# Kernel tuning notes

Measured on AMD Instinct MI355X. Metric: run time of the kernel, lower is better.

The kernel has to match this reference:

```python
import jax, jax.numpy as jnp
import numpy as np

N, P, M, J, H = 32768, 5, 1024, 24, 256
SMPL_THRESH = 0.08


def _rand_transforms(rng, n):
    # random small-angle rotations + small translations -> invertible 4x4 joint transforms
    axis = rng.normal(size=(n, 3))
    axis /= np.linalg.norm(axis, axis=-1, keepdims=True)
    ang = rng.uniform(-0.5, 0.5, size=(n, 1, 1))
    K = np.zeros((n, 3, 3))
    K[:, 0, 1] = -axis[:, 2]; K[:, 0, 2] = axis[:, 1]
    K[:, 1, 0] = axis[:, 2];  K[:, 1, 2] = -axis[:, 0]
    K[:, 2, 0] = -axis[:, 1]; K[:, 2, 1] = axis[:, 0]
    R = np.eye(3)[None] + np.sin(ang) * K + (1.0 - np.cos(ang)) * (K @ K)
    T = np.zeros((n, 4, 4))
    T[:, :3, :3] = R
    T[:, :3, 3] = rng.normal(size=(n, 3)) * 0.1
    T[:, 3, 3] = 1.0
    return T.astype(np.float32)


def setup_inputs() -> dict:
    key = jax.random.key(0)
    ks = jax.random.split(key, 12)
    rng = np.random.default_rng(0)
    pose_pts = jax.random.normal(ks[0], (1, N, 3), jnp.float32) * 0.5
    pose_dirs = jax.random.normal(ks[1], (1, N, 3), jnp.float32)
    pose_dirs = pose_dirs / jnp.linalg.norm(pose_dirs, axis=-1, keepdims=True)
    part_pts = jax.random.normal(ks[2], (P, M, 3), jnp.float32) * 0.5
    part_pbw = jax.nn.softmax(jax.random.normal(ks[3], (P, M, J), jnp.float32), axis=-1)
    A = jnp.asarray(_rand_transforms(rng, J))[None]       # [1,24,4,4]
    big_A = jnp.asarray(_rand_transforms(rng, J))[None]   # [1,24,4,4]
    W1 = jax.random.normal(ks[4], (3, H), jnp.float32) * 0.1
    b1 = jnp.zeros((H,), jnp.float32)
    W2 = jax.random.normal(ks[5], (H, H), jnp.float32) * 0.06
    b2 = jnp.zeros((H,), jnp.float32)
    W3 = jax.random.normal(ks[6], (H, 3), jnp.float32) * 0.06
    b3 = jnp.zeros((3,), jnp.float32)
    lengths2 = jnp.full((P,), M, dtype=jnp.int32)
    return {"pose_pts": pose_pts, "pose_dirs": pose_dirs, "part_pts": part_pts,
            "part_pbw": part_pbw, "A": A, "big_A": big_A,
            "W1": W1, "b1": b1, "W2": W2, "b2": b2, "W3": W3, "b3": b3,
            "lengths2": lengths2}


def _lbs_pipeline(pose_pts, pose_dirs, part_pts, part_pbw, A, big_A,
                  W1, b1, W2, b2, W3, b3, lengths2):
    # ---- KNN (K=1) blend-weight lookup per part (torch.no_grad block) ----
    x = pose_pts[0]                                              # [N,3]
    d2 = (jnp.sum(x * x, -1)[:, None, None]
          - 2.0 * jnp.einsum('nd,pmd->npm', x, part_pts)
          + jnp.sum(part_pts * part_pts, -1)[None])              # [N,P,M]
    valid = jnp.arange(M)[None, :] < lengths2[:, None]           # [P,M]
    d2 = jnp.where(valid[None], jnp.maximum(d2, 0.0), jnp.inf)
    nn = jnp.argmin(d2, axis=-1)                                 # [N,P]
    pnorm = jnp.sqrt(jnp.take_along_axis(d2, nn[..., None], -1)[..., 0])  # [N,P]
    bw = part_pbw[jnp.arange(P)[None, :], nn]                    # [N,P,24]
    bw = jax.lax.stop_gradient(bw)
    pnorm = jax.lax.stop_gradient(pnorm)
    pflag = pnorm < SMPL_THRESH                                  # [N,P]

    # ---- gather-expand: each point assigned to every part ----
    pts_e = jnp.broadcast_to(x[:, None, :], (N, P, 3)).reshape(N * P, 3)
    dirs_e = jnp.broadcast_to(pose_dirs[0][:, None, :], (N, P, 3)).reshape(N * P, 3)
    bw_f = bw.reshape(N * P, J)

    # ---- per-point inverse linear blend skinning ----
    A_bw = jnp.einsum('kj,jxy->kxy', bw_f, A[0])                 # [NP,4,4]
    R_inv = jnp.linalg.inv(A_bw[:, :3, :3])
    tpts = jnp.einsum('kxy,ky->kx', R_inv, pts_e - A_bw[:, :3, 3])
    Ab = jnp.einsum('kj,jxy->kxy', bw_f, big_A[0])               # [NP,4,4]
    Rb = Ab[:, :3, :3]
    init_bigpose = jnp.einsum('kxy,ky->kx', Rb, tpts) + Ab[:, :3, 3]
    tdirs = jnp.einsum('kxy,ky->kx', R_inv, dirs_e)
    tpose_dirs = jnp.einsum('kxy,ky->kx', Rb, tdirs).reshape(1, N, P, 3)

    # ---- tpose deformer (residual MLP, masked by part flag) ----
    h = jax.nn.relu(init_bigpose @ W1 + b1)
    h = jax.nn.relu(h @ W2 + b2)
    resd = 0.05 * jnp.tanh(h @ W3 + b3)
    resd = resd * pflag.reshape(N * P, 1).astype(resd.dtype)
    tpose = (init_bigpose + resd).reshape(1, N, P, 3)
    return (tpose, tpose_dirs, resd.reshape(1, N, P, 3),
            pflag.reshape(1, N, P), init_bigpose[None], pnorm[None])


def reference(pose_pts, pose_dirs, part_pts, part_pbw, A, big_A,
              W1, b1, W2, b2, W3, b3, lengths2):
    return _lbs_pipeline(pose_pts, pose_dirs, part_pts, part_pbw, A, big_A,
                         W1, b1, W2, b2, W3, b3, lengths2)
```

## Files before the change

kernel.cpp:

```cpp
#include <hip/hip_runtime.h>
#include <stdint.h>
#include <math.h>

#define NPTS 32768
#define PP   5
#define MM   1024
#define JJ   24
#define HH   256

#define O0 0
#define O1 491520
#define O2 983040
#define O3 1474560
#define O4 1638400
#define O5 2129920

typedef unsigned short ushort_t;
typedef unsigned int   uint_t;
typedef unsigned long long u64_t;
typedef __attribute__((ext_vector_type(8))) short bf16x8;
typedef __attribute__((ext_vector_type(4))) float f32x4;
typedef __attribute__((ext_vector_type(2))) float f32x2;

__device__ __forceinline__ ushort_t f2bf(float f) {
  union { uint_t i; float f; } v; v.f = f;
  uint_t i = v.i;
  return (ushort_t)((i + 0x7FFFu + ((i >> 16) & 1u)) >> 16);
}
__device__ __forceinline__ uint_t cvt_pk_bf16(float lo, float hi) {
  uint_t r;
  asm("v_cvt_pk_bf16_f32 %0, %1, %2" : "=v"(r) : "v"(lo), "v"(hi));
  return r;
}
__device__ __forceinline__ float tanh_fast(float v) {
  v = fminf(fmaxf(v, -15.f), 15.f);
  float e = __expf(2.f*v);
  return __fdividef(e - 1.f, e + 1.f);
}
__device__ __forceinline__ float dpp_sum16(float x) {
  x += __int_as_float(__builtin_amdgcn_update_dpp(0, __float_as_int(x), 0x108, 0xF, 0xF, true));
  x += __int_as_float(__builtin_amdgcn_update_dpp(0, __float_as_int(x), 0x104, 0xF, 0xF, true));
  x += __int_as_float(__builtin_amdgcn_update_dpp(0, __float_as_int(x), 0x102, 0xF, 0xF, true));
  x += __int_as_float(__builtin_amdgcn_update_dpp(0, __float_as_int(x), 0x101, 0xF, 0xF, true));
  return x;
}

__device__ __forceinline__ void transform_one(
    int n, int p, int nn, float pn, float fl,
    float px, float py, float pz, float dx, float dy, float dz,
    const float* __restrict__ pbw,
    const float4* __restrict__ sA4, const float4* __restrict__ sB4,
    float* __restrict__ out)
{
  const float4* bwr = (const float4*)(pbw + ((size_t)p * MM + nn) * JJ);
  float bw[24];
  #pragma unroll
  for (int q = 0; q < 6; ++q) {
    float4 u = bwr[q];
    bw[q*4+0] = u.x; bw[q*4+1] = u.y; bw[q*4+2] = u.z; bw[q*4+3] = u.w;
  }

  float M1[12], M2[12];
  #pragma unroll
  for (int q = 0; q < 12; ++q) { M1[q] = 0.f; M2[q] = 0.f; }
  #pragma unroll
  for (int j = 0; j < 24; ++j) {
    float w = bw[j];
    float4 a0 = sA4[j*3+0], a1 = sA4[j*3+1], a2 = sA4[j*3+2];
    M1[0]=fmaf(w,a0.x,M1[0]); M1[1]=fmaf(w,a0.y,M1[1]); M1[2]=fmaf(w,a0.z,M1[2]); M1[3]=fmaf(w,a0.w,M1[3]);
    M1[4]=fmaf(w,a1.x,M1[4]); M1[5]=fmaf(w,a1.y,M1[5]); M1[6]=fmaf(w,a1.z,M1[6]); M1[7]=fmaf(w,a1.w,M1[7]);
    M1[8]=fmaf(w,a2.x,M1[8]); M1[9]=fmaf(w,a2.y,M1[9]); M1[10]=fmaf(w,a2.z,M1[10]); M1[11]=fmaf(w,a2.w,M1[11]);
    float4 c0 = sB4[j*3+0], c1 = sB4[j*3+1], c2 = sB4[j*3+2];
    M2[0]=fmaf(w,c0.x,M2[0]); M2[1]=fmaf(w,c0.y,M2[1]); M2[2]=fmaf(w,c0.z,M2[2]); M2[3]=fmaf(w,c0.w,M2[3]);
    M2[4]=fmaf(w,c1.x,M2[4]); M2[5]=fmaf(w,c1.y,M2[5]); M2[6]=fmaf(w,c1.z,M2[6]); M2[7]=fmaf(w,c1.w,M2[7]);
    M2[8]=fmaf(w,c2.x,M2[8]); M2[9]=fmaf(w,c2.y,M2[9]); M2[10]=fmaf(w,c2.z,M2[10]); M2[11]=fmaf(w,c2.w,M2[11]);
  }
  float a=M1[0], b=M1[1], c=M1[2];
  float d=M1[4], e=M1[5], f=M1[6];
  float g=M1[8], h=M1[9], i=M1[10];
  float C00 = e*i - f*h, C01 = c*h - b*i, C02 = b*f - c*e;
  float C10 = f*g - d*i, C11 = a*i - c*g, C12 = c*d - a*f;
  float C20 = d*h - e*g, C21 = b*g - a*h, C22 = a*e - b*d;
  float det = a*C00 + b*C10 + c*C20;
  float rd = 1.0f / det;
  float tx = px - M1[3], ty = py - M1[7], tz = pz - M1[11];
  float t0 = rd * (C00*tx + C01*ty + C02*tz);
  float t1 = rd * (C10*tx + C11*ty + C12*tz);
  float t2 = rd * (C20*tx + C21*ty + C22*tz);
  float i0 = M2[0]*t0 + M2[1]*t1 + M2[2]*t2  + M2[3];
  float i1 = M2[4]*t0 + M2[5]*t1 + M2[6]*t2  + M2[7];
  float i2 = M2[8]*t0 + M2[9]*t1 + M2[10]*t2 + M2[11];
  float d0 = rd * (C00*dx + C01*dy + C02*dz);
  float d1 = rd * (C10*dx + C11*dy + C12*dz);
  float d2 = rd * (C20*dx + C21*dy + C22*dz);
  float e0 = M2[0]*d0 + M2[1]*d1 + M2[2]*d2;
  float e1 = M2[4]*d0 + M2[5]*d1 + M2[6]*d2;
  float e2 = M2[8]*d0 + M2[9]*d1 + M2[10]*d2;

  size_t k = (size_t)n * PP + p;
  out[O1 + k*3+0] = e0; out[O1 + k*3+1] = e1; out[O1 + k*3+2] = e2;
  out[O3 + k] = fl;
  out[O4 + k*3+0] = i0; out[O4 + k*3+1] = i1; out[O4 + k*3+2] = i2;
  out[O5 + k] = pn;
}

__global__ __launch_bounds__(256) void nn_kernel(
    const float* __restrict__ pp0, const float* __restrict__ pp1,
    const float* __restrict__ part_pts, const float* __restrict__ pbw,
    const float* __restrict__ Ag, const float* __restrict__ Bg,
    const int* __restrict__ lengths2,
    const float* __restrict__ W2g, ushort_t* __restrict__ W2bf,
    float* __restrict__ out)
{
  if (blockIdx.x >= 1280) {
    int k = blockIdx.x - 1280;
    int n = threadIdx.x;
    float v = W2g[k*256 + n];
    int kc = k >> 5, quad = (k & 31) >> 3, j = k & 7;
    int tile = n >> 4, lane = quad*16 + (n & 15);
    W2bf[kc*8192 + tile*512 + lane*8 + j] = f2bf(v);
    return;
  }

  __shared__ float4 sXq[256], sYq[256], sZq[256], sWq[256];
  __shared__ float4 sA4[72];
  __shared__ float4 sB4[72];
  int t = threadIdx.x;
  int p  = blockIdx.x >> 8;
  int nb = blockIdx.x & 255;
  int g  = t >> 3;
  int s  = t & 7;
  int n0 = nb*128 + g*4;

  float s0r0 = pp0[0], s0r1 = pp0[1], s0r2 = pp0[2];
  float nrm = s0r0*s0r0 + s0r1*s0r1 + s0r2*s0r2;
  bool c0_is_dirs = fabsf(nrm - 1.0f) < 1e-4f;
  const float* pose_pts  = c0_is_dirs ? pp1 : pp0;
  const float* pose_dirs = c0_is_dirs ? pp0 : pp1;

  {
    #pragma clang fp contract(off)
    float* fX = (float*)sXq; float* fY = (float*)sYq;
    float* fZ = (float*)sZq; float* fW = (float*)sWq;
    for (int i = t; i < MM; i += 256) {
      float x = part_pts[((size_t)p*MM+i)*3+0];
      float y = part_pts[((size_t)p*MM+i)*3+1];
      float z = part_pts[((size_t)p*MM+i)*3+2];
      float yy = ((x*x) + (y*y)) + (z*z);
      fX[i] = x; fY[i] = y; fZ[i] = z; fW[i] = yy;
    }
  }
  for (int i = t; i < 72; i += 256) {
    int l = i*4;
    int j = l / 12, rc = l % 12;
    float4 qa, qb;
    qa.x = Ag[j*16+rc+0]; qa.y = Ag[j*16+rc+1]; qa.z = Ag[j*16+rc+2]; qa.w = Ag[j*16+rc+3];
    qb.x = Bg[j*16+rc+0]; qb.y = Bg[j*16+rc+1]; qb.z = Bg[j*16+rc+2]; qb.w = Bg[j*16+rc+3];
    sA4[i] = qa; sB4[i] = qb;
  }
  int mlen = lengths2[p]; if (mlen > MM) mlen = MM;
  __syncthreads();

  float X[4], Y[4], Z[4];
  f32x2 Xd[4], Yd[4], Zd[4], C2[4];
  {
    #pragma clang fp contract(off)
    const float4* pr = (const float4*)(pose_pts + (size_t)n0*3);
    float4 f0 = pr[0], f1 = pr[1], f2 = pr[2];
    X[0]=f0.x; Y[0]=f0.y; Z[0]=f0.z;
    X[1]=f0.w; Y[1]=f1.x; Z[1]=f1.y;
    X[2]=f1.z; Y[2]=f1.w; Z[2]=f2.x;
    X[3]=f2.y; Y[3]=f2.z; Z[3]=f2.w;
    #pragma unroll
    for (int j = 0; j < 4; ++j) {
      float x2 = ((X[j]*X[j]) + (Y[j]*Y[j])) + (Z[j]*Z[j]);
      Xd[j] = (f32x2){2.0f*X[j], 2.0f*X[j]};
      Yd[j] = (f32x2){2.0f*Y[j], 2.0f*Y[j]};
      Zd[j] = (f32x2){2.0f*Z[j], 2.0f*Z[j]};
      C2[j] = (f32x2){x2, x2};
    }
  }

  float best[4]  = {INFINITY, INFINITY, INFINITY, INFINITY};
  int   kb[4]    = {0, 0, 0, 0};
  int   mbest[4] = {0, 0, 0, 0};
  int   nq = mlen >> 5;
  {
    #pragma clang fp contract(off)
    for (int k = 0; k < nq; ++k) {
      int qi = k*8 + s;
      float4 QX = sXq[qi], QY = sYq[qi], QZ = sZq[qi], QW = sWq[qi];
      f32x2 qx0 = {QX.x, QX.y}, qx1 = {QX.z, QX.w};
      f32x2 qy0 = {QY.x, QY.y}, qy1 = {QY.z, QY.w};
      f32x2 qz0 = {QZ.x, QZ.y}, qz1 = {QZ.z, QZ.w};
      f32x2 qw0 = {QW.x, QW.y}, qw1 = {QW.z, QW.w};
      #pragma unroll
      for (int j = 0; j < 4; ++j) {
        f32x2 dt0 = ((Xd[j]*qx0) + (Yd[j]*qy0)) + (Zd[j]*qz0);
        f32x2 tt0 = (C2[j] - dt0) + qw0;
        f32x2 dt1 = ((Xd[j]*qx1) + (Yd[j]*qy1)) + (Zd[j]*qz1);
        f32x2 tt1 = (C2[j] - dt1) + qw1;
        float e0 = fmaxf(tt0.x, 0.f);
        float e1 = fmaxf(tt0.y, 0.f);
        float e2 = fmaxf(tt1.x, 0.f);
        float e3 = fmaxf(tt1.y, 0.f);
        float m01 = fminf(e0, e1);
        float m23 = fminf(e2, e3);
        float lmin = fminf(m01, m23);
        bool lt = lmin < best[j];
        best[j] = fminf(best[j], lmin);
        kb[j] = lt ? k : kb[j];
      }
    }
    if (nq > 0) {
      #pragma unroll
      for (int j = 0; j < 4; ++j) {
        int qi = kb[j]*8 + s;
        float4 QX = sXq[qi], QY = sYq[qi], QZ = sZq[qi], QW = sWq[qi];
        float dA = ((Xd[j].x*QX.x) + (Yd[j].x*QY.x)) + (Zd[j].x*QZ.x);
        float eA = fmaxf((C2[j].x - dA) + QW.x, 0.f);
        float dB = ((Xd[j].x*QX.y) + (Yd[j].x*QY.y)) + (Zd[j].x*QZ.y);
        float eB = fmaxf((C2[j].x - dB) + QW.y, 0.f);
        float dC = ((Xd[j].x*QX.z) + (Yd[j].x*QY.z)) + (Zd[j].x*QZ.z);
        float eC = fmaxf((C2[j].x - dC) + QW.z, 0.f);
        int e = (eA == best[j]) ? 0 : (eB == best[j]) ? 1 : (eC == best[j]) ? 2 : 3;
        mbest[j] = (kb[j] << 5) + 4*s + e;
      }
    } else {
      #pragma unroll
      for (int j = 0; j < 4; ++j) mbest[j] = 4*s;
    }
    int mb0 = nq << 5;
    if (mb0 < mlen) {
      const float* fX = (const float*)sXq; const float* fY = (const float*)sYq;
      const float* fZ = (const float*)sZq; const float* fW = (const float*)sWq;
      #pragma unroll
      for (int e = 0; e < 4; ++e) {
        int m = mb0 + 4*s + e;
        if (m < mlen) {
          float qx = fX[m], qy = fY[m], qz = fZ[m], qw = fW[m];
          #pragma unroll
          for (int j = 0; j < 4; ++j) {
            float dt2 = ((Xd[j].x*qx) + (Yd[j].x*qy)) + (Zd[j].x*qz);
            float dd = fmaxf((C2[j].x - dt2) + qw, 0.0f);
            bool lt = dd < best[j];
            best[j] = fminf(best[j], dd);
            mbest[j] = lt ? m : mbest[j];
          }
        }
      }
    }
  }

  u64_t pk[4];
  #pragma unroll
  for (int j = 0; j < 4; ++j) {
    pk[j] = ((u64_t)__float_as_uint(best[j]) << 32) | (uint_t)mbest[j];
    u64_t o;
    o = __shfl_xor(pk[j], 1); if (o < pk[j]) pk[j] = o;
    o = __shfl_xor(pk[j], 2); if (o < pk[j]) pk[j] = o;
    o = __shfl_xor(pk[j], 4); if (o < pk[j]) pk[j] = o;
  }

  if (s < 4) {
    u64_t mypk = (s==0) ? pk[0] : (s==1) ? pk[1] : (s==2) ? pk[2] : pk[3];
    float xa = (s==0) ? X[0] : (s==1) ? X[1] : (s==2) ? X[2] : X[3];
    float ya = (s==0) ? Y[0] : (s==1) ? Y[1] : (s==2) ? Y[2] : Y[3];
    float za = (s==0) ? Z[0] : (s==1) ? Z[1] : (s==2) ? Z[2] : Z[3];
    int n = n0 + s;
    int bm = (int)(mypk & 0xFFFFFFFFull);
    float bd = __uint_as_float((uint_t)(mypk >> 32));
    float pn = sqrtf(bd);
    float fl = ((double)pn < 0.08) ? 1.0f : 0.0f;
    float dxa = pose_dirs[n*3+0], dya = pose_dirs[n*3+1], dza = pose_dirs[n*3+2];
    transform_one(n, p, bm, pn, fl, xa, ya, za, dxa, dya, dza, pbw, sA4, sB4, out);
  }
}

__global__ __launch_bounds__(256) void mlp_kernel(
    const float* __restrict__ W1g, const float* __restrict__ b1g,
    const float* __restrict__ b2g, const float* __restrict__ W3g,
    const float* __restrict__ b3g, const ushort_t* __restrict__ W2bf,
    float* __restrict__ out)
{
  __shared__ __align__(16) char smem[25088];
  ushort_t* sH   = (ushort_t*)smem;
  float4*   w1c  = (float4*)(smem + 16384);
  float4*   w3b2 = (float4*)(smem + 20480);
  float4*   sRow = (float4*)(smem + 24576);
  float*    prt  = (float*)smem;

  int t = threadIdx.x;
  int wave = t >> 6, lane = t & 63, quad = lane >> 4, m16 = lane & 15;
  size_t row0 = (size_t)blockIdx.x * 128;

  {
    int c = t;
    w1c[c]  = make_float4(W1g[c], W1g[256+c], W1g[512+c], b1g[c]);
    w3b2[c] = make_float4(W3g[c*3+0], W3g[c*3+1], W3g[c*3+2], b2g[c]);
  }

  #pragma unroll 1
  for (int pass = 0; pass < 4; ++pass) {
    size_t rbase = row0 + pass*32;
    if (t < 32) {
      size_t r = rbase + t;
      sRow[t] = make_float4(out[O4 + r*3+0], out[O4 + r*3+1], out[O4 + r*3+2],
                            out[O3 + r]);
    }
    __syncthreads();

    {
      int q8 = t & 31, rg = t >> 5;
      int kcw = q8 >> 2, qd = q8 & 3;
      int c0 = kcw*32 + qd*8;
      float4 wv[8];
      #pragma unroll
      for (int j = 0; j < 8; ++j) wv[j] = w1c[c0 + j];
      #pragma unroll
      for (int rr = 0; rr < 4; ++rr) {
        int r = rg*4 + rr;
        float4 xyz = sRow[r];
        uint_t u0, u1, u2, u3;
        {
          float4 wA = wv[0], wB = wv[1];
          float hA = fmaxf(fmaf(xyz.z, wA.z, fmaf(xyz.y, wA.y, fmaf(xyz.x, wA.x, wA.w))), 0.f);
          float hB = fmaxf(fmaf(xyz.z, wB.z, fmaf(xyz.y, wB.y, fmaf(xyz.x, wB.x, wB.w))), 0.f);
          u0 = cvt_pk_bf16(hA, hB);
        }
        {
          float4 wA = wv[2], wB = wv[3];
          float hA = fmaxf(fmaf(xyz.z, wA.z, fmaf(xyz.y, wA.y, fmaf(xyz.x, wA.x, wA.w))), 0.f);
          float hB = fmaxf(fmaf(xyz.z, wB.z, fmaf(xyz.y, wB.y, fmaf(xyz.x, wB.x, wB.w))), 0.f);
          u1 = cvt_pk_bf16(hA, hB);
        }
        {
          float4 wA = wv[4], wB = wv[5];
          float hA = fmaxf(fmaf(xyz.z, wA.z, fmaf(xyz.y, wA.y, fmaf(xyz.x, wA.x, wA.w))), 0.f);
          float hB = fmaxf(fmaf(xyz.z, wB.z, fmaf(xyz.y, wB.y, fmaf(xyz.x, wB.x, wB.w))), 0.f);
          u2 = cvt_pk_bf16(hA, hB);
        }
        {
          float4 wA = wv[6], wB = wv[7];
          float hA = fmaxf(fmaf(xyz.z, wA.z, fmaf(xyz.y, wA.y, fmaf(xyz.x, wA.x, wA.w))), 0.f);
          float hB = fmaxf(fmaf(xyz.z, wB.z, fmaf(xyz.y, wB.y, fmaf(xyz.x, wB.x, wB.w))), 0.f);
          u3 = cvt_pk_bf16(hA, hB);
        }
        int mt = r >> 4, r15 = r & 15;
        int l = qd*16 + r15;
        *(uint4*)(&sH[((mt*8 + kcw)*64 + l)*8]) = make_uint4(u0, u1, u2, u3);
      }
    }
    __syncthreads();

    const ushort_t* Wlane = W2bf + (size_t)wave*2048 + lane*8;
    bf16x8 Bcur[4], Bnxt[4];
    #pragma unroll
    for (int q = 0; q < 4; ++q) Bcur[q] = *(const bf16x8*)(Wlane + q*512);

    f32x4 acc[8];
    #pragma unroll
    for (int i = 0; i < 8; ++i) acc[i] = (f32x4){0.f,0.f,0.f,0.f};

    #pragma unroll 1
    for (int kc = 0; kc < 8; ++kc) {
      bf16x8 Af[2];
      #pragma unroll
      for (int mt = 0; mt < 2; ++mt)
        Af[mt] = *(const bf16x8*)(&sH[((mt*8 + kc)*64 + lane)*8]);
      if (kc < 7) {
        #pragma unroll
        for (int q = 0; q < 4; ++q)
          Bnxt[q] = *(const bf16x8*)(Wlane + (kc+1)*8192 + q*512);
      }
      #pragma unroll
      for (int mt = 0; mt < 2; ++mt)
        #pragma unroll
        for (int q = 0; q < 4; ++q)
          acc[mt*4+q] = __builtin_amdgcn_mfma_f32_16x16x32_bf16(Af[mt], Bcur[q], acc[mt*4+q], 0, 0, 0);
      if (kc < 7) {
        #pragma unroll
        for (int q = 0; q < 4; ++q) Bcur[q] = Bnxt[q];
      }
    }
    __syncthreads();

    float4 cvq[4];
    #pragma unroll
    for (int q = 0; q < 4; ++q) cvq[q] = w3b2[(wave*4+q)*16 + m16];

    #pragma unroll
    for (int mt = 0; mt < 2; ++mt) {
      #pragma unroll
      for (int reg = 0; reg < 4; ++reg) {
        float q0 = 0.f, q1 = 0.f, q2 = 0.f;
        #pragma unroll
        for (int q = 0; q < 4; ++q) {
          float h2 = fmaxf(acc[mt*4+q][reg] + cvq[q].w, 0.f);
          q0 = fmaf(h2, cvq[q].x, q0);
          q1 = fmaf(h2, cvq[q].y, q1);
          q2 = fmaf(h2, cvq[q].z, q2);
        }
        q0 = dpp_sum16(q0);
        q1 = dpp_sum16(q1);
        q2 = dpp_sum16(q2);
        if (m16 == 0) {
          int lr = mt*16 + quad*4 + reg;
          prt[(lr*4 + wave)*3 + 0] = q0;
          prt[(lr*4 + wave)*3 + 1] = q1;
          prt[(lr*4 + wave)*3 + 2] = q2;
        }
      }
    }
    __syncthreads();

    if (t < 128) {
      int lr = t >> 2, c = t & 3;
      if (c < 3) {
        float v = ((prt[(lr*4+0)*3+c] + prt[(lr*4+1)*3+c]) + prt[(lr*4+2)*3+c]) + prt[(lr*4+3)*3+c];
        size_t r = rbase + lr;
        float4 ib = sRow[lr];
        float iv = (c == 0) ? ib.x : (c == 1) ? ib.y : ib.z;
        float rr = 0.05f * tanh_fast(v + b3g[c]) * ib.w;
        out[O0 + r*3 + c] = iv + rr;
        out[O2 + r*3 + c] = rr;
      }
    }
    __syncthreads();
  }
}

extern "C" void kernel_launch(void* const* d_in, const int* in_sizes, int n_in,
                              void* d_out, int out_size, void* d_ws, size_t ws_size,
                              hipStream_t stream) {
  (void)out_size; (void)ws_size;
  const int want[13] = {98304, 98304, 15360, 122880, 384, 384, 768, 256, 65536, 256, 768, 3, 5};
  int idx[13];
  bool used[64] = {false};
  for (int L = 0; L < 13; ++L) {
    idx[L] = -1;
    for (int s = 0; s < n_in && s < 64; ++s) {
      if (!used[s] && in_sizes[s] == want[L]) { idx[L] = s; used[s] = true; break; }
    }
    if (idx[L] < 0) idx[L] = L;
  }
  const float* pp0       = (const float*)d_in[idx[0]];
  const float* pp1       = (const float*)d_in[idx[1]];
  const float* part_pts  = (const float*)d_in[idx[2]];
  const float* part_pbw  = (const float*)d_in[idx[3]];
  const float* A         = (const float*)d_in[idx[4]];
  const float* bigA      = (const float*)d_in[idx[5]];
  const float* W1        = (const float*)d_in[idx[6]];
  const float* b1        = (const float*)d_in[idx[7]];
  const float* W2        = (const float*)d_in[idx[8]];
  const float* b2        = (const float*)d_in[idx[9]];
  const float* W3        = (const float*)d_in[idx[10]];
  const float* b3        = (const float*)d_in[idx[11]];
  const int*   lengths2  = (const int*)d_in[idx[12]];
  float* out = (float*)d_out;
  ushort_t* W2bf = (ushort_t*)d_ws;

  nn_kernel<<<1536, 256, 0, stream>>>(pp0, pp1, part_pts, part_pbw,
                                      A, bigA, lengths2, W2, W2bf, out);
  mlp_kernel<<<1280, 256, 0, stream>>>(W1, b1, b2, W3, b3, W2bf, out);
}
```

Measured before the change: 170.2 us.

## Process 64 rows per MLP block in one pass instead of four 32-row passes

The MLP kernel now handles 64 rows per block in a single pass rather than looping over four 32-row passes of a 128-row block, and the grid doubles to 2560 blocks. Each W2 fragment loaded from global memory now feeds four M-tiles instead of two, doubling reuse per load, and the per-pass barriers are removed. The layer-1 compute is re-mapped so each thread handles one row and eight column groups. The cost is 16 accumulator vectors per thread, which raises register pressure, and more blocks each reloading W1/W3 into shared memory.

```diff
diff --git a/kernel.cpp b/kernel.cpp
--- a/kernel.cpp
+++ b/kernel.cpp
@@ -283,150 +283,138 @@
     const float* __restrict__ b3g, const ushort_t* __restrict__ W2bf,
     float* __restrict__ out)
 {
-  __shared__ __align__(16) char smem[25088];
-  ushort_t* sH   = (ushort_t*)smem;
-  float4*   w1c  = (float4*)(smem + 16384);
-  float4*   w3b2 = (float4*)(smem + 20480);
-  float4*   sRow = (float4*)(smem + 24576);
-  float*    prt  = (float*)smem;
+  __shared__ ushort_t sH[4*8*512];
+  __shared__ float4 w1c[256];
+  __shared__ float4 w3b2[256];
+  __shared__ float4 sRow[64];
+  __shared__ float  prt[64][4][3];
 
   int t = threadIdx.x;
   int wave = t >> 6, lane = t & 63, quad = lane >> 4, m16 = lane & 15;
-  size_t row0 = (size_t)blockIdx.x * 128;
+  size_t row0 = (size_t)blockIdx.x * 64;
 
   {
     int c = t;
     w1c[c]  = make_float4(W1g[c], W1g[256+c], W1g[512+c], b1g[c]);
     w3b2[c] = make_float4(W3g[c*3+0], W3g[c*3+1], W3g[c*3+2], b2g[c]);
-  }
-
-  #pragma unroll 1
-  for (int pass = 0; pass < 4; ++pass) {
-    size_t rbase = row0 + pass*32;
-    if (t < 32) {
-      size_t r = rbase + t;
+    if (t < 64) {
+      size_t r = row0 + t;
       sRow[t] = make_float4(out[O4 + r*3+0], out[O4 + r*3+1], out[O4 + r*3+2],
                             out[O3 + r]);
     }
-    __syncthreads();
-
-    {
-      int q8 = t & 31, rg = t >> 5;
-      int kcw = q8 >> 2, qd = q8 & 3;
+  }
+  __syncthreads();
+
+  {
+    int r = t & 63;
+    float4 xyz = sRow[r];
+    int mt = r >> 4, r15 = r & 15;
+    #pragma unroll
+    for (int j = 0; j < 8; ++j) {
+      int o = wave*8 + j;
+      int kcw = o >> 2, qd = o & 3;
       int c0 = kcw*32 + qd*8;
-      float4 wv[8];
-      #pragma unroll
-      for (int j = 0; j < 8; ++j) wv[j] = w1c[c0 + j];
-      #pragma unroll
-      for (int rr = 0; rr < 4; ++rr) {
-        int r = rg*4 + rr;
-        float4 xyz = sRow[r];
-        uint_t u0, u1, u2, u3;
-        {
-          float4 wA = wv[0], wB = wv[1];
-          float hA = fmaxf(fmaf(xyz.z, wA.z, fmaf(xyz.y, wA.y, fmaf(xyz.x, wA.x, wA.w))), 0.f);
-          float hB = fmaxf(fmaf(xyz.z, wB.z, fmaf(xyz.y, wB.y, fmaf(xyz.x, wB.x, wB.w))), 0.f);
-          u0 = cvt_pk_bf16(hA, hB);
-        }
-        {
-          float4 wA = wv[2], wB = wv[3];
-          float hA = fmaxf(fmaf(xyz.z, wA.z, fmaf(xyz.y, wA.y, fmaf(xyz.x, wA.x, wA.w))), 0.f);
-          float hB = fmaxf(fmaf(xyz.z, wB.z, fmaf(xyz.y, wB.y, fmaf(xyz.x, wB.x, wB.w))), 0.f);
-          u1 = cvt_pk_bf16(hA, hB);
-        }
-        {
-          float4 wA = wv[4], wB = wv[5];
-          float hA = fmaxf(fmaf(xyz.z, wA.z, fmaf(xyz.y, wA.y, fmaf(xyz.x, wA.x, wA.w))), 0.f);
-          float hB = fmaxf(fmaf(xyz.z, wB.z, fmaf(xyz.y, wB.y, fmaf(xyz.x, wB.x, wB.w))), 0.f);
-          u2 = cvt_pk_bf16(hA, hB);
-        }
-        {
-          float4 wA = wv[6], wB = wv[7];
-          float hA = fmaxf(fmaf(xyz.z, wA.z, fmaf(xyz.y, wA.y, fmaf(xyz.x, wA.x, wA.w))), 0.f);
-          float hB = fmaxf(fmaf(xyz.z, wB.z, fmaf(xyz.y, wB.y, fmaf(xyz.x, wB.x, wB.w))), 0.f);
-          u3 = cvt_pk_bf16(hA, hB);
-        }
-        int mt = r >> 4, r15 = r & 15;
-        int l = qd*16 + r15;
-        *(uint4*)(&sH[((mt*8 + kcw)*64 + l)*8]) = make_uint4(u0, u1, u2, u3);
-      }
-    }
-    __syncthreads();
-
-    const ushort_t* Wlane = W2bf + (size_t)wave*2048 + lane*8;
-    bf16x8 Bcur[4], Bnxt[4];
+      uint_t u0, u1, u2, u3;
+      {
+        float4 wA = w1c[c0 + 0], wB = w1c[c0 + 1];
+        float hA = fmaxf(fmaf(xyz.z, wA.z, fmaf(xyz.y, wA.y, fmaf(xyz.x, wA.x, wA.w))), 0.f);
+        float hB = fmaxf(fmaf(xyz.z, wB.z, fmaf(xyz.y, wB.y, fmaf(xyz.x, wB.x, wB.w))), 0.f);
+        u0 = cvt_pk_bf16(hA, hB);
+      }
+      {
+        float4 wA = w1c[c0 + 2], wB = w1c[c0 + 3];
+        float hA = fmaxf(fmaf(xyz.z, wA.z, fmaf(xyz.y, wA.y, fmaf(xyz.x, wA.x, wA.w))), 0.f);
+        float hB = fmaxf(fmaf(xyz.z, wB.z, fmaf(xyz.y, wB.y, fmaf(xyz.x, wB.x, wB.w))), 0.f);
+        u1 = cvt_pk_bf16(hA, hB);
+      }
+      {
+        float4 wA = w1c[c0 + 4], wB = w1c[c0 + 5];
+        float hA = fmaxf(fmaf(xyz.z, wA.z, fmaf(xyz.y, wA.y, fmaf(xyz.x, wA.x, wA.w))), 0.f);
+        float hB = fmaxf(fmaf(xyz.z, wB.z, fmaf(xyz.y, wB.y, fmaf(xyz.x, wB.x, wB.w))), 0.f);
+        u2 = cvt_pk_bf16(hA, hB);
+      }
+      {
+        float4 wA = w1c[c0 + 6], wB = w1c[c0 + 7];
+        float hA = fmaxf(fmaf(xyz.z, wA.z, fmaf(xyz.y, wA.y, fmaf(xyz.x, wA.x, wA.w))), 0.f);
+        float hB = fmaxf(fmaf(xyz.z, wB.z, fmaf(xyz.y, wB.y, fmaf(xyz.x, wB.x, wB.w))), 0.f);
+        u3 = cvt_pk_bf16(hA, hB);
+      }
+      *(uint4*)(&sH[((mt*8 + kcw)*64 + qd*16 + r15)*8]) = make_uint4(u0, u1, u2, u3);
+    }
+  }
+  __syncthreads();
+
+  const ushort_t* Wlane = W2bf + (size_t)wave*2048 + lane*8;
+  bf16x8 Bcur[4], Bnxt[4];
+  #pragma unroll
+  for (int q = 0; q < 4; ++q) Bcur[q] = *(const bf16x8*)(Wlane + q*512);
+
+  f32x4 acc[16];
+  #pragma unroll
+  for (int i = 0; i < 16; ++i) acc[i] = (f32x4){0.f,0.f,0.f,0.f};
+
+  #pragma unroll 1
+  for (int kc = 0; kc < 8; ++kc) {
+    bf16x8 Af[4];
     #pragma unroll
-    for (int q = 0; q < 4; ++q) Bcur[q] = *(const bf16x8*)(Wlane + q*512);
-
-    f32x4 acc[8];
+    for (int mt = 0; mt < 4; ++mt)
+      Af[mt] = *(const bf16x8*)(&sH[((mt*8 + kc)*64 + lane)*8]);
+    if (kc < 7) {
+      #pragma unroll
+      for (int q = 0; q < 4; ++q)
+        Bnxt[q] = *(const bf16x8*)(Wlane + (kc+1)*8192 + q*512);
+    }
     #pragma unroll
-    for (int i = 0; i < 8; ++i) acc[i] = (f32x4){0.f,0.f,0.f,0.f};
-
-    #pragma unroll 1
-    for (int kc = 0; kc < 8; ++kc) {
-      bf16x8 Af[2];
-      #pragma unroll
-      for (int mt = 0; mt < 2; ++mt)
-        Af[mt] = *(const bf16x8*)(&sH[((mt*8 + kc)*64 + lane)*8]);
-      if (kc < 7) {
-        #pragma unroll
-        for (int q = 0; q < 4; ++q)
-          Bnxt[q] = *(const bf16x8*)(Wlane + (kc+1)*8192 + q*512);
-      }
-      #pragma unroll
-      for (int mt = 0; mt < 2; ++mt)
-        #pragma unroll
-        for (int q = 0; q < 4; ++q)
-          acc[mt*4+q] = __builtin_amdgcn_mfma_f32_16x16x32_bf16(Af[mt], Bcur[q], acc[mt*4+q], 0, 0, 0);
-      if (kc < 7) {
-        #pragma unroll
-        for (int q = 0; q < 4; ++q) Bcur[q] = Bnxt[q];
-      }
-    }
-    __syncthreads();
-
-    float4 cvq[4];
+    for (int mt = 0; mt < 4; ++mt)
+      #pragma unroll
+      for (int q = 0; q < 4; ++q)
+        acc[mt*4+q] = __builtin_amdgcn_mfma_f32_16x16x32_bf16(Af[mt], Bcur[q], acc[mt*4+q], 0, 0, 0);
+    if (kc < 7) {
+      #pragma unroll
+      for (int q = 0; q < 4; ++q) Bcur[q] = Bnxt[q];
+    }
+  }
+
+  float4 cvq[4];
+  #pragma unroll
+  for (int q = 0; q < 4; ++q) cvq[q] = w3b2[(wave*4+q)*16 + m16];
+
+  #pragma unroll
+  for (int mt = 0; mt < 4; ++mt) {
     #pragma unroll
-    for (int q = 0; q < 4; ++q) cvq[q] = w3b2[(wave*4+q)*16 + m16];
-
-    #pragma unroll
-    for (int mt = 0; mt < 2; ++mt) {
-      #pragma unroll
-      for (int reg = 0; reg < 4; ++reg) {
-        float q0 = 0.f, q1 = 0.f, q2 = 0.f;
-        #pragma unroll
-        for (int q = 0; q < 4; ++q) {
-          float h2 = fmaxf(acc[mt*4+q][reg] + cvq[q].w, 0.f);
-          q0 = fmaf(h2, cvq[q].x, q0);
-          q1 = fmaf(h2, cvq[q].y, q1);
-          q2 = fmaf(h2, cvq[q].z, q2);
-        }
-        q0 = dpp_sum16(q0);
-        q1 = dpp_sum16(q1);
-        q2 = dpp_sum16(q2);
-        if (m16 == 0) {
-          int lr = mt*16 + quad*4 + reg;
-          prt[(lr*4 + wave)*3 + 0] = q0;
-          prt[(lr*4 + wave)*3 + 1] = q1;
-          prt[(lr*4 + wave)*3 + 2] = q2;
-        }
-      }
-    }
-    __syncthreads();
-
-    if (t < 128) {
-      int lr = t >> 2, c = t & 3;
-      if (c < 3) {
-        float v = ((prt[(lr*4+0)*3+c] + prt[(lr*4+1)*3+c]) + prt[(lr*4+2)*3+c]) + prt[(lr*4+3)*3+c];
-        size_t r = rbase + lr;
-        float4 ib = sRow[lr];
-        float iv = (c == 0) ? ib.x : (c == 1) ? ib.y : ib.z;
-        float rr = 0.05f * tanh_fast(v + b3g[c]) * ib.w;
-        out[O0 + r*3 + c] = iv + rr;
-        out[O2 + r*3 + c] = rr;
-      }
-    }
-    __syncthreads();
+    for (int reg = 0; reg < 4; ++reg) {
+      float q0 = 0.f, q1 = 0.f, q2 = 0.f;
+      #pragma unroll
+      for (int q = 0; q < 4; ++q) {
+        float h2 = fmaxf(acc[mt*4+q][reg] + cvq[q].w, 0.f);
+        q0 = fmaf(h2, cvq[q].x, q0);
+        q1 = fmaf(h2, cvq[q].y, q1);
+        q2 = fmaf(h2, cvq[q].z, q2);
+      }
+      q0 = dpp_sum16(q0);
+      q1 = dpp_sum16(q1);
+      q2 = dpp_sum16(q2);
+      if (m16 == 0) {
+        int lr = mt*16 + quad*4 + reg;
+        prt[lr][wave][0] = q0;
+        prt[lr][wave][1] = q1;
+        prt[lr][wave][2] = q2;
+      }
+    }
+  }
+  __syncthreads();
+
+  {
+    int lr = t >> 2, c = t & 3;
+    if (c < 3) {
+      float v = ((prt[lr][0][c] + prt[lr][1][c]) + prt[lr][2][c]) + prt[lr][3][c];
+      size_t r = row0 + lr;
+      float4 ib = sRow[lr];
+      float iv = (c == 0) ? ib.x : (c == 1) ? ib.y : ib.z;
+      float rr = 0.05f * tanh_fast(v + b3g[c]) * ib.w;
+      out[O0 + r*3 + c] = iv + rr;
+      out[O2 + r*3 + c] = rr;
+    }
   }
 }
 
@@ -462,5 +450,5 @@
 
   nn_kernel<<<1536, 256, 0, stream>>>(pp0, pp1, part_pts, part_pbw,
                                       A, bigA, lengths2, W2, W2bf, out);
-  mlp_kernel<<<1280, 256, 0, stream>>>(W1, b1, b2, W3, b3, W2bf, out);
-}
+  mlp_kernel<<<2560, 256, 0, stream>>>(W1, b1, b2, W3, b3, W2bf, out);
+}
```

After: 159.9 us (median of 2 runs). -6.0%, faster.
